# Kernel tuning notes

Measured on AMD Instinct MI355X. Metric: run time of the kernel, lower is better.

## Reference

```python
import jax, jax.numpy as jnp
import numpy as np

B, C, H, W = 16, 256, 48, 160
BASELINE = 0.54
REL_ELEV = 1.65
H_MEAN = 1.535


def setup_inputs() -> dict:
    key = jax.random.key(0)
    k = jax.random.split(key, 5)
    features = jax.random.normal(k[0], (B, C, H, W), dtype=jnp.float32)
    # realistic KITTI-style P2 (full-resolution intrinsics; forward divides rows 0:2 by 16)
    base = np.zeros((3, 4), np.float32)
    base[0, 0] = 721.5; base[1, 1] = 721.5
    base[0, 2] = 609.5; base[1, 2] = 172.8
    base[2, 2] = 1.0;   base[1, 3] = 0.2
    P2 = jnp.asarray(base)[None] + 0.5 * jax.random.uniform(k[1], (B, 3, 4), dtype=jnp.float32)
    w_disp = 0.05 * jax.random.normal(k[2], (1, C, 3, 3), dtype=jnp.float32)  # disp_create conv3x3
    b_disp = jnp.zeros((1,), jnp.float32)
    w_ext = 0.05 * jax.random.normal(k[3], (C, C + 1), dtype=jnp.float32)     # extract conv1x1 (O,I)
    b_ext = jnp.zeros((C,), jnp.float32)
    alpha = 0.5 * jnp.ones((1,), jnp.float32)  # nn.Parameter (init 0.0; nonzero to exercise path)
    return {"features": features, "P2": P2, "w_disp": w_disp, "b_disp": b_disp,
            "w_ext": w_ext, "b_ext": b_ext, "alpha": alpha}


def _grid_sample_border(feat, gx, gy):
    """Bilinear grid_sample, padding_mode='border', align_corners=True.
    feat: (B,C1,H,W); gx, gy: (B,H,W) in [-1,1]."""
    Bs, C1, Hs, Ws = feat.shape
    ix = jnp.clip((gx + 1.0) * 0.5 * (Ws - 1), 0.0, Ws - 1)
    iy = jnp.clip((gy + 1.0) * 0.5 * (Hs - 1), 0.0, Hs - 1)
    ix0 = jnp.floor(ix); iy0 = jnp.floor(iy)
    ix1 = jnp.minimum(ix0 + 1.0, Ws - 1); iy1 = jnp.minimum(iy0 + 1.0, Hs - 1)
    wx = (ix - ix0).reshape(Bs, 1, -1)
    wy = (iy - iy0).reshape(Bs, 1, -1)
    flat = feat.reshape(Bs, C1, Hs * Ws)

    def gather(f, yq, xq):
        idx = (yq * Ws + xq).astype(jnp.int32).reshape(-1)
        return f[:, idx]  # (C1, H*W)

    g = jax.vmap(gather)
    v00 = g(flat, iy0, ix0); v01 = g(flat, iy0, ix1)
    v10 = g(flat, iy1, ix0); v11 = g(flat, iy1, ix1)
    out = (v00 * (1 - wx) * (1 - wy) + v01 * wx * (1 - wy)
           + v10 * (1 - wx) * wy + v11 * wx * wy)
    return out.reshape(Bs, C1, Hs, Ws)


def reference(features, P2, w_disp, b_disp, w_ext, b_ext, alpha):
    x = features
    Bs = x.shape[0]
    P2 = P2.at[:, 0:2].set(P2[:, 0:2] / 16.0)
    # disp_create: conv3x3 -> tanh, then detach-scaled
    d = jax.lax.conv_general_dilated(x, w_disp, (1, 1), 'SAME',
                                     dimension_numbers=('NCHW', 'OIHW', 'NCHW'))
    d = jnp.tanh(d + b_disp[None, :, None, None])
    disp = 0.1 * (0.05 * d + 0.95 * jax.lax.stop_gradient(d))  # (B,1,H,W)

    yy = jnp.arange(H, dtype=jnp.float32)[None, :, None]  # (1,H,1): row index
    fy = P2[:, 1:2, 1:2]; cy = P2[:, 1:2, 2:3]; Ty = P2[:, 1:2, 3:4]  # (B,1,1)
    disparity = jax.nn.relu(fy * BASELINE * (yy - cy)
                            / (jnp.abs(fy * REL_ELEV + Ty) + 1e-10))  # (B,H,1)
    disparity = jnp.broadcast_to(disparity, (Bs, H, W))

    x_base = jnp.broadcast_to(jnp.linspace(-1.0, 1.0, W, dtype=jnp.float32)[None, None, :], (Bs, H, W))
    y_base = jnp.linspace(-1.0, 1.0, H, dtype=jnp.float32)[None, :, None]  # (1,H,1)
    y_shifts_base = jax.nn.relu(H_MEAN * (yy - cy) / (2.0 * (REL_ELEV - 0.5 * H_MEAN))) / (H * 0.5)
    y_shifts = y_shifts_base + disp[:, 0]  # (B,H,W)
    gy = y_base + y_shifts

    feats = jnp.concatenate([disparity[:, None], x], axis=1)  # (B,C+1,H,W)
    samp = _grid_sample_border(feats, x_base, gy)
    out = jnp.einsum('oc,bchw->bohw', w_ext, samp) + b_ext[None, :, None, None]
    return jax.nn.relu(x + out * alpha[0])
```

## Files before the change

### kernel.cpp

```cpp
#include <hip/hip_runtime.h>
#include <stdint.h>

#define NB 16
#define NC 256
#define NH 48
#define NW 160
#define HW (NH*NW)
#define NP (NB*HW)

static __device__ __forceinline__ unsigned short f2bf(float f){
  union { float f; uint32_t u; } v; v.f = f;
  uint32_t u = v.u;
  uint32_t r = (u + 0x7FFFu + ((u >> 16) & 1u)) >> 16;
  return (unsigned short)r;
}
static __device__ __forceinline__ float bf2f(unsigned short h){
  union { float f; uint32_t u; } v; v.u = ((uint32_t)h) << 16; return v.f;
}

__global__ __launch_bounds__(256) void kw_conv(const float* __restrict__ w_ext,
                                               const float* __restrict__ w_disp,
                                               unsigned short* __restrict__ Wb,
                                               unsigned short* __restrict__ Wtap){
  if (blockIdx.x < 256){
    int idx = blockIdx.x * 256 + threadIdx.x;
    int o = idx >> 8, c = idx & 255;
    Wb[idx] = f2bf(w_ext[o * 257 + 1 + c]);
  } else {
    int c = threadIdx.x;
    #pragma unroll
    for (int m = 0; m < 16; ++m){
      float v = (m < 9) ? w_disp[c * 9 + m] : 0.f;
      Wtap[m * 256 + c] = f2bf(v);
    }
  }
}

typedef __attribute__((ext_vector_type(8))) short bf16x8;
typedef __attribute__((ext_vector_type(4))) float f32x4;

__global__ __launch_bounds__(256) void kb_gemm(
    const float* __restrict__ x,
    const unsigned short* __restrict__ Wb,
    const unsigned short* __restrict__ Wtap,
    unsigned short* __restrict__ U,
    float* __restrict__ T)
{
  __shared__ __align__(16) unsigned short smem[2][4 * 512];
  int bx = blockIdx.x;
  int b  = bx / 120;
  int nt = bx - b * 120;
  int p0 = nt * 64;

  int tid  = threadIdx.x;
  int lane = tid & 63;
  int w    = tid >> 6;
  int l15 = lane & 15;
  int lq  = lane >> 4;

  int sn  = tid & 63;
  int skq = tid >> 6;
  const float* xbase = x + ((size_t)b * NC) * HW + p0 + sn;
  const int swroff = (sn >> 4) * 512 + ((sn & 15) + skq * 16) * 8;

  f32x4 zero = {0.f, 0.f, 0.f, 0.f};
  f32x4 acc[4][4];
  f32x4 acct[4];
  #pragma unroll
  for (int mi = 0; mi < 4; ++mi){
    acct[mi] = zero;
    #pragma unroll
    for (int ni = 0; ni < 4; ++ni) acc[mi][ni] = zero;
  }

  float r0[8], r1[8];
  #pragma unroll
  for (int j = 0; j < 8; ++j) r0[j] = xbase[(size_t)(skq * 8 + j) * HW];
  #pragma unroll
  for (int j = 0; j < 8; ++j) r1[j] = xbase[(size_t)(32 + skq * 8 + j) * HW];
  {
    unsigned short h[8];
    #pragma unroll
    for (int j = 0; j < 8; ++j) h[j] = f2bf(r0[j]);
    *(bf16x8*)(smem[0] + swroff) = *(bf16x8*)h;
  }
  asm volatile("s_waitcnt lgkmcnt(0)" ::: "memory");
  __builtin_amdgcn_sched_barrier(0);
  __builtin_amdgcn_s_barrier();
  __builtin_amdgcn_sched_barrier(0);

#define KB_ITER(T_, RCUR, RNXT)                                               \
  {                                                                           \
    constexpr int t_ = (T_);                                                  \
    if (t_ + 2 < 8) {                                                         \
      _Pragma("unroll")                                                       \
      for (int j = 0; j < 8; ++j)                                             \
        RCUR[j] = xbase[(size_t)((t_ + 2) * 32 + skq * 8 + j) * HW];          \
    }                                                                         \
    bf16x8 af[4], bg[4];                                                      \
    _Pragma("unroll")                                                         \
    for (int ni = 0; ni < 4; ++ni)                                            \
      bg[ni] = *(const bf16x8*)(smem[t_ & 1] + ni * 512 + lane * 8);          \
    _Pragma("unroll")                                                         \
    for (int mi = 0; mi < 4; ++mi)                                            \
      af[mi] = *(const bf16x8*)(Wb + (size_t)(w * 64 + mi * 16 + l15) * 256   \
                                + t_ * 32 + lq * 8);                          \
    _Pragma("unroll")                                                         \
    for (int mi = 0; mi < 4; ++mi)                                            \
      _Pragma("unroll")                                                       \
      for (int ni = 0; ni < 4; ++ni)                                          \
        acc[mi][ni] = __builtin_amdgcn_mfma_f32_16x16x32_bf16(af[mi], bg[ni], \
                                                      acc[mi][ni], 0, 0, 0);  \
    if (w == 0) {                                                             \
      bf16x8 at = *(const bf16x8*)(Wtap + (size_t)l15 * 256 + t_ * 32 + lq * 8); \
      _Pragma("unroll")                                                       \
      for (int ni = 0; ni < 4; ++ni)                                          \
        acct[ni] = __builtin_amdgcn_mfma_f32_16x16x32_bf16(at, bg[ni],        \
                                                       acct[ni], 0, 0, 0);    \
    }                                                                         \
    if (t_ + 1 < 8) {                                                         \
      unsigned short h[8];                                                    \
      _Pragma("unroll")                                                       \
      for (int j = 0; j < 8; ++j) h[j] = f2bf(RNXT[j]);                       \
      *(bf16x8*)(smem[(t_ + 1) & 1] + swroff) = *(bf16x8*)h;                  \
      asm volatile("s_waitcnt lgkmcnt(0)" ::: "memory");                      \
      __builtin_amdgcn_sched_barrier(0);                                      \
      __builtin_amdgcn_s_barrier();                                           \
      __builtin_amdgcn_sched_barrier(0);                                      \
    }                                                                         \
  }

  KB_ITER(0, r0, r1)
  KB_ITER(1, r1, r0)
  KB_ITER(2, r0, r1)
  KB_ITER(3, r1, r0)
  KB_ITER(4, r0, r1)
  KB_ITER(5, r1, r0)
  KB_ITER(6, r0, r1)
  KB_ITER(7, r1, r0)
#undef KB_ITER

  #pragma unroll
  for (int mi = 0; mi < 4; ++mi){
    #pragma unroll
    for (int ni = 0; ni < 4; ++ni){
      int o = w * 64 + mi * 16 + lq * 4;
      int n = ni * 16 + l15;
      size_t base = ((size_t)(b * NC + o)) * HW + p0 + n;
      #pragma unroll
      for (int r = 0; r < 4; ++r)
        U[base + (size_t)r * HW] = f2bf(acc[mi][ni][r]);
    }
  }
  if (w == 0){
    #pragma unroll
    for (int ni = 0; ni < 4; ++ni){
      int n = ni * 16 + l15;
      #pragma unroll
      for (int r = 0; r < 4; ++r){
        int k = lq * 4 + r;
        if (k < 9)
          T[(size_t)k * NP + (size_t)b * HW + p0 + n] = acct[ni][r];
      }
    }
  }
}

__global__ __launch_bounds__(256) void kp_grid(
    const float* __restrict__ P2, const float* __restrict__ b_disp,
    const float* __restrict__ T, float4* __restrict__ pre)
{
  int p = blockIdx.x * 256 + threadIdx.x;
  int b  = p / HW;
  int hw = p - b * HW;
  int y  = hw / NW;
  int xx = hw - y * NW;

  float d = 0.f;
  #pragma unroll
  for (int ky = 0; ky < 3; ++ky){
    int yy2 = y + ky - 1;
    if (yy2 < 0 || yy2 >= NH) continue;
    #pragma unroll
    for (int kx = 0; kx < 3; ++kx){
      int xx2 = xx + kx - 1;
      if (xx2 < 0 || xx2 >= NW) continue;
      d += T[(size_t)(ky * 3 + kx) * NP + b * HW + yy2 * NW + xx2];
    }
  }
  float th = tanhf(d + b_disp[0]);

  float fy = P2[b * 12 + 5] * 0.0625f;
  float cy = P2[b * 12 + 6] * 0.0625f;
  float Ty = P2[b * 12 + 7] * 0.0625f;

  float ysb   = fmaxf(1.535f * ((float)y - cy) / 1.765f, 0.f) * (1.f / 24.f);
  float ybase = -1.f + (float)y * (2.f / 47.f);
  float gy = ybase + ysb + 0.1f * th;
  float iy = fminf(fmaxf((gy + 1.f) * 0.5f * 47.f, 0.f), 47.f);
  float fiy0 = floorf(iy);
  float wy = iy - fiy0;
  int iy0 = (int)fiy0;
  int iy1 = min(iy0 + 1, 47);

  float inv_den = 1.f / (fabsf(fy * 1.65f + Ty) + 1e-10f);
  float dr0 = fmaxf(fy * 0.54f * ((float)iy0 - cy) * inv_den, 0.f);
  float dr1 = fmaxf(fy * 0.54f * ((float)iy1 - cy) * inv_den, 0.f);
  float dlerp = (1.f - wy) * dr0 + wy * dr1;

  float4 pr;
  pr.x = wy; pr.y = dlerp;
  pr.z = __int_as_float(iy0 * NW + xx);
  pr.w = __int_as_float(iy1 * NW + xx);
  pre[p] = pr;
}

__global__ __launch_bounds__(256) void kc_epilogue(
    const float* __restrict__ x, const float* __restrict__ w_ext,
    const float* __restrict__ b_ext, const float* __restrict__ alpha,
    const unsigned short* __restrict__ U, const float4* __restrict__ pre,
    float* __restrict__ out)
{
  int bx = blockIdx.x;
  int ptile = bx >> 3;
  int cg    = bx & 7;
  int p = ptile * 256 + threadIdx.x;
  int b  = p / HW;
  int hw = p - b * HW;

  float4 pr = pre[p];
  float wy    = pr.x;
  float dlerp = pr.y;
  int off0 = __float_as_int(pr.z);
  int off1 = __float_as_int(pr.w);
  float w1 = 1.f - wy;
  float al = alpha[0];

  size_t base0 = (size_t)(b * NC) * HW;
  const unsigned short* Ub = U + base0;
  const float* xb = x + base0 + hw;
  float* ob = out + base0 + hw;

  int o0 = cg * 32;
  #pragma unroll 4
  for (int o = o0; o < o0 + 32; ++o){
    float u0 = bf2f(Ub[(size_t)o * HW + off0]);
    float u1 = bf2f(Ub[(size_t)o * HW + off1]);
    float val = w1 * u0 + wy * u1 + w_ext[o * 257] * dlerp + b_ext[o];
    float r = xb[(size_t)o * HW] + al * val;
    ob[(size_t)o * HW] = fmaxf(r, 0.f);
  }
}

extern "C" void kernel_launch(void* const* d_in, const int* in_sizes, int n_in,
                              void* d_out, int out_size, void* d_ws, size_t ws_size,
                              hipStream_t stream) {
  const float* features = (const float*)d_in[0];
  const float* P2       = (const float*)d_in[1];
  const float* w_disp   = (const float*)d_in[2];
  const float* b_disp   = (const float*)d_in[3];
  const float* w_ext    = (const float*)d_in[4];
  const float* b_ext    = (const float*)d_in[5];
  const float* alpha    = (const float*)d_in[6];
  float* out = (float*)d_out;

  char* ws = (char*)d_ws;
  const size_t U_bytes   = (size_t)NP * 256 * 2;
  const size_t T_bytes   = (size_t)9 * NP * 4;
  const size_t pre_bytes = (size_t)NP * 16;
  unsigned short* U    = (unsigned short*)ws;
  float*          T    = (float*)(ws + U_bytes);
  float4*         pre  = (float4*)(ws + U_bytes + T_bytes);
  unsigned short* Wb   = (unsigned short*)(ws + U_bytes + T_bytes + pre_bytes);
  unsigned short* Wtap = Wb + 256 * 256;

  hipLaunchKernelGGL(kw_conv,     dim3(257),  dim3(256), 0, stream, w_ext, w_disp, Wb, Wtap);
  hipLaunchKernelGGL(kb_gemm,     dim3(1920), dim3(256), 0, stream, features, Wb, Wtap, U, T);
  hipLaunchKernelGGL(kp_grid,     dim3(480),  dim3(256), 0, stream, P2, b_disp, T, pre);
  hipLaunchKernelGGL(kc_epilogue, dim3(3840), dim3(256), 0, stream,
                     features, w_ext, b_ext, alpha, U, pre, out);
}
```

Baseline: 316.6 us.

## Pre-swizzle bf16 weights into MFMA fragment order and prefetch A fragments

The weight-conversion kernel now writes Wb and Wtap in the exact per-lane MFMA fragment order, so each lane loads a contiguous 16-byte chunk instead of a strided row read. The GEMM kernel double-buffers the A (weight) fragments in registers, loading the next k-step's fragments one iteration ahead to hide global-load latency behind the MFMAs. This costs more VGPRs, which may reduce occupancy, and enlarges the prep grid to cover the expanded tap layout.

Result: faster. 305.8 us (-3.4%).

```diff
diff --git a/kernel.cpp b/kernel.cpp
--- a/kernel.cpp
+++ b/kernel.cpp
@@ -20,19 +20,26 @@
 
 __global__ __launch_bounds__(256) void kw_conv(const float* __restrict__ w_ext,
                                                const float* __restrict__ w_disp,
-                                               unsigned short* __restrict__ Wb,
-                                               unsigned short* __restrict__ Wtap){
+                                               unsigned short* __restrict__ WbF,
+                                               unsigned short* __restrict__ WtapF){
+  int d = blockIdx.x * 256 + threadIdx.x;
   if (blockIdx.x < 256){
-    int idx = blockIdx.x * 256 + threadIdx.x;
-    int o = idx >> 8, c = idx & 255;
-    Wb[idx] = f2bf(w_ext[o * 257 + 1 + c]);
+    int j  = d & 7;
+    int lane = (d >> 3) & 63;
+    int mi = (d >> 9) & 3;
+    int w  = (d >> 11) & 3;
+    int ks = d >> 13;
+    int m = w * 64 + mi * 16 + (lane & 15);
+    int k = ks * 32 + (lane >> 4) * 8 + j;
+    WbF[d] = f2bf(w_ext[m * 257 + 1 + k]);
   } else {
-    int c = threadIdx.x;
-    #pragma unroll
-    for (int m = 0; m < 16; ++m){
-      float v = (m < 9) ? w_disp[c * 9 + m] : 0.f;
-      Wtap[m * 256 + c] = f2bf(v);
-    }
+    int d2 = d - 65536;
+    int j  = d2 & 7;
+    int lane = (d2 >> 3) & 63;
+    int ks = d2 >> 9;
+    int tap = lane & 15;
+    int k = ks * 32 + (lane >> 4) * 8 + j;
+    WtapF[d2] = (tap < 9) ? f2bf(w_disp[k * 9 + tap]) : (unsigned short)0;
   }
 }
 
@@ -74,10 +81,17 @@
   }
 
   float r0[8], r1[8];
+  bf16x8 afA[4], afB[4];
+  bf16x8 atA = {0,0,0,0,0,0,0,0}, atB = {0,0,0,0,0,0,0,0};
   #pragma unroll
   for (int j = 0; j < 8; ++j) r0[j] = xbase[(size_t)(skq * 8 + j) * HW];
   #pragma unroll
   for (int j = 0; j < 8; ++j) r1[j] = xbase[(size_t)(32 + skq * 8 + j) * HW];
+  #pragma unroll
+  for (int mi = 0; mi < 4; ++mi)
+    afA[mi] = *(const bf16x8*)(Wb + ((0 * 16 + w * 4 + mi) << 9) + lane * 8);
+  if (w == 0)
+    atA = *(const bf16x8*)(Wtap + (0 << 9) + lane * 8);
   {
     unsigned short h[8];
     #pragma unroll
@@ -89,7 +103,7 @@
   __builtin_amdgcn_s_barrier();
   __builtin_amdgcn_sched_barrier(0);
 
-#define KB_ITER(T_, RCUR, RNXT)                                               \
+#define KB_ITER(T_, RCUR, RNXT, AFC, AFN, ATC, ATN)                           \
   {                                                                           \
     constexpr int t_ = (T_);                                                  \
     if (t_ + 2 < 8) {                                                         \
@@ -97,25 +111,28 @@
       for (int j = 0; j < 8; ++j)                                             \
         RCUR[j] = xbase[(size_t)((t_ + 2) * 32 + skq * 8 + j) * HW];          \
     }                                                                         \
-    bf16x8 af[4], bg[4];                                                      \
+    if (t_ + 1 < 8) {                                                         \
+      _Pragma("unroll")                                                       \
+      for (int mi = 0; mi < 4; ++mi)                                          \
+        AFN[mi] = *(const bf16x8*)(Wb + (((t_ + 1) * 16 + w * 4 + mi) << 9)   \
+                                   + lane * 8);                               \
+      if (w == 0)                                                             \
+        ATN = *(const bf16x8*)(Wtap + ((t_ + 1) << 9) + lane * 8);            \
+    }                                                                         \
+    bf16x8 bg[4];                                                             \
     _Pragma("unroll")                                                         \
     for (int ni = 0; ni < 4; ++ni)                                            \
       bg[ni] = *(const bf16x8*)(smem[t_ & 1] + ni * 512 + lane * 8);          \
     _Pragma("unroll")                                                         \
     for (int mi = 0; mi < 4; ++mi)                                            \
-      af[mi] = *(const bf16x8*)(Wb + (size_t)(w * 64 + mi * 16 + l15) * 256   \
-                                + t_ * 32 + lq * 8);                          \
-    _Pragma("unroll")                                                         \
-    for (int mi = 0; mi < 4; ++mi)                                            \
       _Pragma("unroll")                                                       \
       for (int ni = 0; ni < 4; ++ni)                                          \
-        acc[mi][ni] = __builtin_amdgcn_mfma_f32_16x16x32_bf16(af[mi], bg[ni], \
+        acc[mi][ni] = __builtin_amdgcn_mfma_f32_16x16x32_bf16(AFC[mi], bg[ni],\
                                                       acc[mi][ni], 0, 0, 0);  \
     if (w == 0) {                                                             \
-      bf16x8 at = *(const bf16x8*)(Wtap + (size_t)l15 * 256 + t_ * 32 + lq * 8); \
       _Pragma("unroll")                                                       \
       for (int ni = 0; ni < 4; ++ni)                                          \
-        acct[ni] = __builtin_amdgcn_mfma_f32_16x16x32_bf16(at, bg[ni],        \
+        acct[ni] = __builtin_amdgcn_mfma_f32_16x16x32_bf16(ATC, bg[ni],       \
                                                        acct[ni], 0, 0, 0);    \
     }                                                                         \
     if (t_ + 1 < 8) {                                                         \
@@ -130,14 +147,14 @@
     }                                                                         \
   }
 
-  KB_ITER(0, r0, r1)
-  KB_ITER(1, r1, r0)
-  KB_ITER(2, r0, r1)
-  KB_ITER(3, r1, r0)
-  KB_ITER(4, r0, r1)
-  KB_ITER(5, r1, r0)
-  KB_ITER(6, r0, r1)
-  KB_ITER(7, r1, r0)
+  KB_ITER(0, r0, r1, afA, afB, atA, atB)
+  KB_ITER(1, r1, r0, afB, afA, atB, atA)
+  KB_ITER(2, r0, r1, afA, afB, atA, atB)
+  KB_ITER(3, r1, r0, afB, afA, atB, atA)
+  KB_ITER(4, r0, r1, afA, afB, atA, atB)
+  KB_ITER(5, r1, r0, afB, afA, atB, atA)
+  KB_ITER(6, r0, r1, afA, afB, atA, atB)
+  KB_ITER(7, r1, r0, afB, afA, atB, atA)
 #undef KB_ITER
 
   #pragma unroll
@@ -274,7 +291,7 @@
   unsigned short* Wb   = (unsigned short*)(ws + U_bytes + T_bytes + pre_bytes);
   unsigned short* Wtap = Wb + 256 * 256;
 
-  hipLaunchKernelGGL(kw_conv,     dim3(257),  dim3(256), 0, stream, w_ext, w_disp, Wb, Wtap);
+  hipLaunchKernelGGL(kw_conv,     dim3(272),  dim3(256), 0, stream, w_ext, w_disp, Wb, Wtap);
   hipLaunchKernelGGL(kb_gemm,     dim3(1920), dim3(256), 0, stream, features, Wb, Wtap, U, T);
   hipLaunchKernelGGL(kp_grid,     dim3(480),  dim3(256), 0, stream, P2, b_disp, T, pre);
   hipLaunchKernelGGL(kc_epilogue, dim3(3840), dim3(256), 0, stream,
```
